# Performance work log

Hardware: AMD Instinct MI355X
Metric: run time of the kernel (lower is better)

The kernel has to match this reference:

```python
import jax, jax.numpy as jnp
import numpy as np

N = 100000   # nodes
E = 200000   # edges
B = 2048     # graphs
D = 256      # embed_dim
L = 5        # gnn layers
NUM_ATOM = 500
NUM_CHI = 500
NUM_BOND_TYPE = 5
NUM_BOND_DIR = 3
BN_EPS = 1e-5


def setup_inputs() -> dict:
    key = jax.random.key(0)
    ks = jax.random.split(key, 20)

    def xavier(k, shape):
        fan_in, fan_out = shape[-2], shape[-1]
        lim = float(np.sqrt(6.0 / (fan_in + fan_out)))
        return jax.random.uniform(k, shape, jnp.float32, -lim, lim)

    inp = {}
    inp["x"] = jax.random.randint(ks[0], (N, 2), 0, NUM_CHI, dtype=jnp.int32)
    inp["edge_index"] = jax.random.randint(ks[1], (2, E), 0, N, dtype=jnp.int32)
    inp["edge_attr"] = jax.random.randint(ks[2], (E, 2), 0, NUM_BOND_DIR, dtype=jnp.int32)
    inp["batch"] = jnp.sort(jax.random.randint(ks[3], (N,), 0, B, dtype=jnp.int32))

    # node embeddings
    inp["x_emb1"] = xavier(ks[4], (NUM_ATOM, D))
    inp["x_emb2"] = xavier(ks[5], (NUM_CHI, D))
    # per-layer edge embeddings (stacked over L layers)
    inp["edge_emb1"] = xavier(ks[6], (L, NUM_BOND_TYPE, D))
    inp["edge_emb2"] = xavier(ks[7], (L, NUM_BOND_DIR, D))
    # per-layer GINE MLP: Linear(D, 2D) -> ReLU -> Linear(2D, D)
    inp["W1"] = xavier(ks[8], (L, D, 2 * D))
    inp["b1"] = jnp.zeros((L, 2 * D), jnp.float32)
    inp["W2"] = xavier(ks[9], (L, 2 * D, D))
    inp["b2"] = jnp.zeros((L, D), jnp.float32)
    # per-layer BatchNorm affine params
    inp["bn_g"] = jnp.ones((L, D), jnp.float32)
    inp["bn_b"] = jnp.zeros((L, D), jnp.float32)
    # output head: Linear(D, D//2) -> Softplus -> Linear(D//2, 2)
    inp["Wo1"] = xavier(ks[10], (D, D // 2))
    inp["bo1"] = jnp.zeros((D // 2,), jnp.float32)
    inp["Wo2"] = xavier(ks[11], (D // 2, 2))
    inp["bo2"] = jnp.zeros((2,), jnp.float32)
    return inp


def reference(x, edge_index, edge_attr, batch,
              x_emb1, x_emb2, edge_emb1, edge_emb2,
              W1, b1, W2, b2, bn_g, bn_b,
              Wo1, bo1, Wo2, bo2):
    n = x.shape[0]
    src, dst = edge_index[0], edge_index[1]
    bt, bd = edge_attr[:, 0], edge_attr[:, 1]

    # initial node features
    h = x_emb1[x[:, 0]] + x_emb2[x[:, 1]]  # [N, D]

    for l in range(L):
        # edge embeddings for real edges
        e = edge_emb1[l][bt] + edge_emb2[l][bd]          # [E, D]
        # self-loop edges carry attr (4, 0)
        self_e = edge_emb1[l][4] + edge_emb2[l][0]       # [D]
        # message = x_j + edge_attr, scatter-add to destination; self-loops add h + self_e
        agg = jax.ops.segment_sum(h[src] + e, dst, num_segments=n) + h + self_e
        # GINE update MLP
        z = jax.nn.relu(agg @ W1[l] + b1[l]) @ W2[l] + b2[l]
        # BatchNorm1d (training-mode batch statistics, biased variance)
        mu = z.mean(axis=0)
        var = z.var(axis=0)
        z = (z - mu) / jnp.sqrt(var + BN_EPS) * bn_g[l] + bn_b[l]
        h = jax.nn.relu(z)  # dropout=0 -> identity

    # global mean pool over graphs
    cnt = jax.ops.segment_sum(jnp.ones((n,), h.dtype), batch, num_segments=B)
    pooled = jax.ops.segment_sum(h, batch, num_segments=B) / jnp.maximum(cnt, 1.0)[:, None]

    # output head (y.size(0) != 2 so proj_head is skipped)
    out = jax.nn.softplus(pooled @ Wo1 + bo1) @ Wo2 + bo2  # [B, 2]
    return out
```

## Files before the change

kernel.cpp:

```cpp
#include <hip/hip_runtime.h>

#define NNODES 100000
#define NEDGES 200000
#define NB     2048
#define DIM    256
#define NLAYERS 5
#define NSB    98

typedef __bf16 bf16x8 __attribute__((ext_vector_type(8)));
typedef float  f32x4  __attribute__((ext_vector_type(4)));

__device__ __forceinline__ float bf2f(unsigned short u) {
    union { unsigned u; float f; } v; v.u = ((unsigned)u) << 16; return v.f;
}
__device__ __forceinline__ unsigned short f2bf(float f) {
    union { float f; unsigned u; } v; v.f = f;
    unsigned r = v.u + 0x7fff + ((v.u >> 16) & 1);
    return (unsigned short)(r >> 16);
}
__device__ __forceinline__ float4 loadZ4(const unsigned short* z, size_t row, int ch) {
    ushort4 u = *(const ushort4*)&z[row * DIM + ch];
    float4 r; r.x = bf2f(u.x); r.y = bf2f(u.y); r.z = bf2f(u.z); r.w = bf2f(u.w); return r;
}

__global__ void zero_i32(int* __restrict__ p, int n) {
    int i = blockIdx.x * 256 + threadIdx.x;
    if (i < n) p[i] = 0;
}

__global__ void transpose_w(const float* __restrict__ W,
                            unsigned short* __restrict__ Wt, int K, int Nw) {
    int l = blockIdx.y;
    int t = blockIdx.x * 256 + threadIdx.x;
    int total = K * Nw;
    if (t >= total) return;
    int k = t / Nw, n = t % Nw;
    Wt[(size_t)l * total + (size_t)n * K + k] = f2bf(W[(size_t)l * total + t]);
}

__global__ void build_etab(const float* __restrict__ ee1, const float* __restrict__ ee2,
                           float* __restrict__ etab) {
    int l = blockIdx.y, c = blockIdx.x, d = threadIdx.x;
    etab[((size_t)l * 15 + c) * DIM + d] =
        ee1[((size_t)l * 5 + c / 3) * DIM + d] + ee2[((size_t)l * 3 + c % 3) * DIM + d];
}

__global__ void csr_hist(const int* __restrict__ ei, int* __restrict__ deg) {
    int j = blockIdx.x * 256 + threadIdx.x;
    if (j < NEDGES) atomicAdd(&deg[ei[NEDGES + j]], 1);
}
__global__ __launch_bounds__(1024) void scan_blk(const int* __restrict__ deg,
                                                 int* __restrict__ rowptr,
                                                 int* __restrict__ bsum) {
    __shared__ int s[1024];
    int b = blockIdx.x, t = threadIdx.x, i = b * 1024 + t;
    s[t] = (i < NNODES) ? deg[i] : 0;
    __syncthreads();
    #pragma unroll
    for (int off = 1; off < 1024; off <<= 1) {
        int u = (t >= off) ? s[t - off] : 0;
        __syncthreads();
        s[t] += u;
        __syncthreads();
    }
    if (i < NNODES) rowptr[i + 1] = s[t];
    if (t == 1023) bsum[b] = s[1023];
}
__global__ void scan_partials(int* __restrict__ bsum) {
    if (threadIdx.x == 0) {
        int acc = 0;
        for (int k = 0; k < NSB; ++k) { acc += bsum[k]; bsum[k] = acc; }
    }
}
__global__ void scan_add(int* __restrict__ rowptr, const int* __restrict__ bsum) {
    int b = blockIdx.x, t = threadIdx.x, i = b * 1024 + t;
    if (b > 0 && i < NNODES) rowptr[i + 1] += bsum[b - 1];
    if (b == 0 && t == 0) rowptr[0] = 0;
}
__global__ void csr_fill(const int* __restrict__ ei, const int* __restrict__ ea,
                         const int* __restrict__ rowptr, int* __restrict__ deg,
                         int* __restrict__ esrc, int* __restrict__ eattr) {
    int j = blockIdx.x * 256 + threadIdx.x;
    if (j >= NEDGES) return;
    int d = ei[NEDGES + j];
    int pos = atomicSub(&deg[d], 1) - 1;
    int slot = rowptr[d] + pos;
    esrc[slot] = ei[j];
    eattr[slot] = ea[2 * j] * 3 + ea[2 * j + 1];
}

__global__ void seg_starts(const int* __restrict__ batch, int* __restrict__ start) {
    int g = blockIdx.x * 256 + threadIdx.x;
    if (g > NB) return;
    int lo = 0, hi = NNODES;
    while (lo < hi) { int mid = (lo + hi) >> 1; if (batch[mid] < g) lo = mid + 1; else hi = mid; }
    start[g] = lo;
}

template <int MODE>
__global__ __launch_bounds__(256) void gather_k(const unsigned short* __restrict__ z,
                                                const int* __restrict__ x,
                                                const float* __restrict__ xe1,
                                                const float* __restrict__ xe2,
                                                const float* __restrict__ statsP,
                                                const float* __restrict__ g_,
                                                const float* __restrict__ b_,
                                                float* __restrict__ statsZ,
                                                const float* __restrict__ etab_l,
                                                const int* __restrict__ rowptr,
                                                const int* __restrict__ esrc,
                                                const int* __restrict__ eattr,
                                                unsigned short* __restrict__ agg) {
    if (blockIdx.x == 0) { statsZ[threadIdx.x] = 0.f; statsZ[256 + threadIdx.x] = 0.f; }
    int i = blockIdx.x * 4 + (threadIdx.x >> 6);
    int lane = threadIdx.x & 63, ch = lane * 4;

    float4 a4, c4;
    if (MODE == 1) {
        float4 s4 = *(const float4*)&statsP[ch];
        float4 q4 = *(const float4*)&statsP[256 + ch];
        float4 g4 = *(const float4*)&g_[ch];
        float4 b4 = *(const float4*)&b_[ch];
        const float invN = 1.0f / (float)NNODES;
        float mux = s4.x * invN, muy = s4.y * invN, muz = s4.z * invN, muw = s4.w * invN;
        a4.x = g4.x * rsqrtf(q4.x * invN - mux * mux + 1e-5f);
        a4.y = g4.y * rsqrtf(q4.y * invN - muy * muy + 1e-5f);
        a4.z = g4.z * rsqrtf(q4.z * invN - muz * muz + 1e-5f);
        a4.w = g4.w * rsqrtf(q4.w * invN - muw * muw + 1e-5f);
        c4.x = b4.x - mux * a4.x; c4.y = b4.y - muy * a4.y;
        c4.z = b4.z - muz * a4.z; c4.w = b4.w - muw * a4.w;
    }

    auto hrow = [&](int row) -> float4 {
        if (MODE == 0) {
            int i0 = x[2 * row], i1 = x[2 * row + 1];
            float4 u = *(const float4*)&xe1[(size_t)i0 * DIM + ch];
            float4 v = *(const float4*)&xe2[(size_t)i1 * DIM + ch];
            return make_float4(u.x + v.x, u.y + v.y, u.z + v.z, u.w + v.w);
        } else {
            float4 h = loadZ4(z, (size_t)row, ch);
            h.x = fmaxf(h.x * a4.x + c4.x, 0.f); h.y = fmaxf(h.y * a4.y + c4.y, 0.f);
            h.z = fmaxf(h.z * a4.z + c4.z, 0.f); h.w = fmaxf(h.w * a4.w + c4.w, 0.f);
            return h;
        }
    };

    float4 se = *(const float4*)&etab_l[12 * DIM + ch];
    float4 hv = hrow(i);
    float4 acc = make_float4(hv.x + se.x, hv.y + se.y, hv.z + se.z, hv.w + se.w);

    int r0 = rowptr[i], r1 = rowptr[i + 1];
    int e = r0;
    for (; e + 2 <= r1; e += 2) {
        int s0 = esrc[e], c0 = eattr[e];
        int s1 = esrc[e + 1], c1 = eattr[e + 1];
        float4 h0 = hrow(s0);
        float4 h1 = hrow(s1);
        float4 e0 = *(const float4*)&etab_l[c0 * DIM + ch];
        float4 e1 = *(const float4*)&etab_l[c1 * DIM + ch];
        acc.x += h0.x + e0.x + h1.x + e1.x; acc.y += h0.y + e0.y + h1.y + e1.y;
        acc.z += h0.z + e0.z + h1.z + e1.z; acc.w += h0.w + e0.w + h1.w + e1.w;
    }
    if (e < r1) {
        int s0 = esrc[e], c0 = eattr[e];
        float4 h0 = hrow(s0);
        float4 e0 = *(const float4*)&etab_l[c0 * DIM + ch];
        acc.x += h0.x + e0.x; acc.y += h0.y + e0.y;
        acc.z += h0.z + e0.z; acc.w += h0.w + e0.w;
    }
    ushort4 o; o.x = f2bf(acc.x); o.y = f2bf(acc.y); o.z = f2bf(acc.z); o.w = f2bf(acc.w);
    *(ushort4*)&agg[(size_t)i * DIM + ch] = o;
}

__global__ __launch_bounds__(512, 6) void mlp64(const unsigned short* __restrict__ agg,
                                                const unsigned short* __restrict__ Wt1,
                                                const float* __restrict__ b1,
                                                const unsigned short* __restrict__ Wt2,
                                                const float* __restrict__ b2,
                                                unsigned short* __restrict__ z,
                                                float* __restrict__ stats) {
    __shared__ unsigned short As[64 * 264];
    __shared__ unsigned short Ts[64 * 136];

    const int rowBase = blockIdx.x * 64;
    const int tid = threadIdx.x;
    const int lane = tid & 63, w = tid >> 6;
    const int lrow = lane & 15, lq = lane >> 4;

    #pragma unroll
    for (int c = tid; c < 64 * 32; c += 512) {
        int r = c >> 5, cc = c & 31;
        int row = rowBase + r; if (row >= NNODES) row = NNODES - 1;
        *(uint4*)&As[r * 264 + cc * 8] = *(const uint4*)&agg[(size_t)row * DIM + cc * 8];
    }
    f32x4 acc2[4][2]{};
    __syncthreads();

    #pragma unroll
    for (int q = 0; q < 4; ++q) {
        f32x4 acc1[4]{};
        const unsigned short* w1p = &Wt1[(size_t)(q * 128 + w * 16 + lrow) * DIM];
        #pragma unroll
        for (int kk = 0; kk < 8; ++kk) {
            const int kc = kk * 32 + lq * 8;
            bf16x8 b = *(const bf16x8*)&w1p[kc];
            bf16x8 a[4];
            #pragma unroll
            for (int mi = 0; mi < 4; ++mi)
                a[mi] = *(const bf16x8*)&As[(mi * 16 + lrow) * 264 + kc];
            #pragma unroll
            for (int mi = 0; mi < 4; ++mi)
                acc1[mi] = __builtin_amdgcn_mfma_f32_16x16x32_bf16(a[mi], b, acc1[mi], 0, 0, 0);
        }
        if (q > 0) __syncthreads();
        {
            int col = w * 16 + lrow;
            float bv = b1[q * 128 + col];
            #pragma unroll
            for (int mi = 0; mi < 4; ++mi)
                #pragma unroll
                for (int r = 0; r < 4; ++r)
                    Ts[(mi * 16 + lq * 4 + r) * 136 + col] = f2bf(fmaxf(acc1[mi][r] + bv, 0.f));
        }
        __syncthreads();
        #pragma unroll
        for (int kk = 0; kk < 4; ++kk) {
            const int kc = kk * 32 + lq * 8;
            bf16x8 a[4], b[2];
            #pragma unroll
            for (int mi = 0; mi < 4; ++mi)
                a[mi] = *(const bf16x8*)&Ts[(mi * 16 + lrow) * 136 + kc];
            #pragma unroll
            for (int ni = 0; ni < 2; ++ni)
                b[ni] = *(const bf16x8*)&Wt2[(size_t)(w * 32 + ni * 16 + lrow) * (2 * DIM) + q * 128 + kc];
            #pragma unroll
            for (int mi = 0; mi < 4; ++mi)
                #pragma unroll
                for (int ni = 0; ni < 2; ++ni)
                    acc2[mi][ni] = __builtin_amdgcn_mfma_f32_16x16x32_bf16(a[mi], b[ni], acc2[mi][ni], 0, 0, 0);
        }
    }

    #pragma unroll
    for (int ni = 0; ni < 2; ++ni) {
        int col = w * 32 + ni * 16 + lrow;
        float bv = b2[col];
        float s = 0.f, q = 0.f;
        #pragma unroll
        for (int mi = 0; mi < 4; ++mi)
            #pragma unroll
            for (int r = 0; r < 4; ++r) {
                int row = rowBase + mi * 16 + lq * 4 + r;
                if (row < NNODES) {
                    float v = acc2[mi][ni][r] + bv;
                    z[(size_t)row * DIM + col] = f2bf(v);
                    s += v; q += v * v;
                }
            }
        s += __shfl_xor(s, 16); s += __shfl_xor(s, 32);
        q += __shfl_xor(q, 16); q += __shfl_xor(q, 32);
        if (lq == 0) {
            atomicAdd(&stats[col], s);
            atomicAdd(&stats[DIM + col], q);
        }
    }
}

__global__ __launch_bounds__(256) void pool_seg(const unsigned short* __restrict__ z,
                                                const float* __restrict__ statsP,
                                                const float* __restrict__ g_,
                                                const float* __restrict__ b_,
                                                const int* __restrict__ start,
                                                float* __restrict__ pooled) {
    int g = blockIdx.x, ch = threadIdx.x;
    float mu = statsP[ch] / (float)NNODES;
    float var = statsP[256 + ch] / (float)NNODES - mu * mu;
    float a = g_[ch] * rsqrtf(var + 1e-5f);
    float c = b_[ch] - mu * a;
    int r0 = start[g], r1 = start[g + 1];
    float s = 0.f;
    for (int i = r0; i < r1; ++i)
        s += fmaxf(bf2f(z[(size_t)i * DIM + ch]) * a + c, 0.f);
    pooled[(size_t)g * DIM + ch] = s / fmaxf((float)(r1 - r0), 1.f);
}

__global__ __launch_bounds__(128) void head_mlp(const float* __restrict__ pooled,
                                                const float* __restrict__ Wo1,
                                                const float* __restrict__ bo1,
                                                const float* __restrict__ Wo2,
                                                const float* __restrict__ bo2,
                                                float* __restrict__ out) {
    __shared__ float p[DIM];
    __shared__ float r0[128], r1[128];
    int g = blockIdx.x, j = threadIdx.x;
    for (int k = j; k < DIM; k += 128) p[k] = pooled[(size_t)g * DIM + k];
    __syncthreads();
    float acc = bo1[j];
    for (int k = 0; k < DIM; ++k) acc += p[k] * Wo1[k * 128 + j];
    float sp = (acc > 20.f) ? acc : log1pf(expf(acc));
    r0[j] = sp * Wo2[j * 2 + 0];
    r1[j] = sp * Wo2[j * 2 + 1];
    __syncthreads();
    for (int s = 64; s > 0; s >>= 1) {
        if (j < s) { r0[j] += r0[j + s]; r1[j] += r1[j + s]; }
        __syncthreads();
    }
    if (j == 0) {
        out[g * 2 + 0] = r0[0] + bo2[0];
        out[g * 2 + 1] = r1[0] + bo2[1];
    }
}

extern "C" void kernel_launch(void* const* d_in, const int* in_sizes, int n_in,
                              void* d_out, int out_size, void* d_ws, size_t ws_size,
                              hipStream_t stream) {
    (void)in_sizes; (void)n_in; (void)out_size;
    const int* x     = (const int*)d_in[0];
    const int* ei    = (const int*)d_in[1];
    const int* ea    = (const int*)d_in[2];
    const int* batch = (const int*)d_in[3];
    const float* xe1 = (const float*)d_in[4];
    const float* xe2 = (const float*)d_in[5];
    const float* ee1 = (const float*)d_in[6];
    const float* ee2 = (const float*)d_in[7];
    const float* W1  = (const float*)d_in[8];
    const float* b1  = (const float*)d_in[9];
    const float* W2  = (const float*)d_in[10];
    const float* b2  = (const float*)d_in[11];
    const float* bng = (const float*)d_in[12];
    const float* bnb = (const float*)d_in[13];
    const float* Wo1 = (const float*)d_in[14];
    const float* bo1 = (const float*)d_in[15];
    const float* Wo2 = (const float*)d_in[16];
    const float* bo2 = (const float*)d_in[17];
    float* out = (float*)d_out;

    if (ws_size < 112000000ull) return;

    char* ws = (char*)d_ws;
    size_t off = 0;
    auto alloc = [&](size_t bytes) { void* p = ws + off; off += (bytes + 255) & ~255ull; return p; };
    unsigned short* z   = (unsigned short*)alloc((size_t)NNODES * DIM * 2);
    unsigned short* agg = (unsigned short*)alloc((size_t)NNODES * DIM * 2);
    unsigned short* Wt1 = (unsigned short*)alloc((size_t)NLAYERS * DIM * 2 * DIM * 2);
    unsigned short* Wt2 = (unsigned short*)alloc((size_t)NLAYERS * DIM * 2 * DIM * 2);
    float* etab         = (float*)alloc((size_t)NLAYERS * 15 * DIM * 4);
    float* stats        = (float*)alloc(2 * 512 * 4);
    float* pooled       = (float*)alloc((size_t)NB * DIM * 4);
    int* gstart         = (int*)alloc((size_t)(NB + 1) * 4);
    int* rowptr         = (int*)alloc((size_t)(NNODES + 1) * 4);
    int* deg            = (int*)alloc((size_t)NNODES * 4);
    int* esrc           = (int*)alloc((size_t)NEDGES * 4);
    int* eattr          = (int*)alloc((size_t)NEDGES * 4);
    int* bsum           = (int*)alloc((size_t)NSB * 4);

    const int WTOT = DIM * 2 * DIM;

    transpose_w<<<dim3((WTOT + 255) / 256, NLAYERS), 256, 0, stream>>>(W1, Wt1, DIM, 2 * DIM);
    transpose_w<<<dim3((WTOT + 255) / 256, NLAYERS), 256, 0, stream>>>(W2, Wt2, 2 * DIM, DIM);
    build_etab<<<dim3(15, NLAYERS), DIM, 0, stream>>>(ee1, ee2, etab);

    zero_i32<<<(NNODES + 255) / 256, 256, 0, stream>>>(deg, NNODES);
    csr_hist<<<(NEDGES + 255) / 256, 256, 0, stream>>>(ei, deg);
    scan_blk<<<NSB, 1024, 0, stream>>>(deg, rowptr, bsum);
    scan_partials<<<1, 64, 0, stream>>>(bsum);
    scan_add<<<NSB, 1024, 0, stream>>>(rowptr, bsum);
    csr_fill<<<(NEDGES + 255) / 256, 256, 0, stream>>>(ei, ea, rowptr, deg, esrc, eattr);
    seg_starts<<<(NB + 1 + 255) / 256, 256, 0, stream>>>(batch, gstart);

    for (int l = 0; l < NLAYERS; ++l) {
        float* statsP = stats + ((l + 1) & 1) * 512;
        float* statsC = stats + (l & 1) * 512;
        if (l == 0)
            gather_k<0><<<NNODES / 4, 256, 0, stream>>>(z, x, xe1, xe2, statsP, bng, bnb, statsC,
                                                        etab, rowptr, esrc, eattr, agg);
        else
            gather_k<1><<<NNODES / 4, 256, 0, stream>>>(z, x, xe1, xe2, statsP,
                                                        bng + (size_t)(l - 1) * DIM, bnb + (size_t)(l - 1) * DIM,
                                                        statsC, etab + (size_t)l * 15 * DIM,
                                                        rowptr, esrc, eattr, agg);
        mlp64<<<(NNODES + 63) / 64, 512, 0, stream>>>(agg, Wt1 + (size_t)l * WTOT, b1 + l * 2 * DIM,
                                                      Wt2 + (size_t)l * WTOT, b2 + l * DIM, z, statsC);
    }

    pool_seg<<<NB, DIM, 0, stream>>>(z, stats + ((NLAYERS - 1) & 1) * 512,
                                     bng + (size_t)(NLAYERS - 1) * DIM, bnb + (size_t)(NLAYERS - 1) * DIM,
                                     gstart, pooled);
    head_mlp<<<NB, 128, 0, stream>>>(pooled, Wo1, bo1, Wo2, bo2, out);
}
```

Before: 1.101 ms.

## Fuse neighbor gather into MLP kernel with ping-pong node buffers

Merges the per-layer gather/aggregate kernel into the MLP kernel. Each 512-thread block now aggregates its 64 rows straight into shared memory instead of writing and re-reading a bf16 agg buffer. Node features ping-pong between two buffers, because one layer's gathers read the previous z while other blocks write the new z. Stats use a 3-slot rotation so the slot being zeroed, read and accumulated never collide. This removes one full N×D round trip through memory and one launch per layer, but the gather now runs at the MLP kernel's occupancy and cannot overlap with the GEMM phase inside a block.

```diff
diff --git a/kernel.cpp b/kernel.cpp
--- a/kernel.cpp
+++ b/kernel.cpp
@@ -26,6 +26,10 @@
 __global__ void zero_i32(int* __restrict__ p, int n) {
     int i = blockIdx.x * 256 + threadIdx.x;
     if (i < n) p[i] = 0;
+}
+__global__ void zero_f32(float* __restrict__ p, int n) {
+    int i = blockIdx.x * 256 + threadIdx.x;
+    if (i < n) p[i] = 0.f;
 }
 
 __global__ void transpose_w(const float* __restrict__ W,
@@ -98,87 +102,24 @@
 }
 
 template <int MODE>
-__global__ __launch_bounds__(256) void gather_k(const unsigned short* __restrict__ z,
-                                                const int* __restrict__ x,
-                                                const float* __restrict__ xe1,
-                                                const float* __restrict__ xe2,
-                                                const float* __restrict__ statsP,
-                                                const float* __restrict__ g_,
-                                                const float* __restrict__ b_,
-                                                float* __restrict__ statsZ,
-                                                const float* __restrict__ etab_l,
-                                                const int* __restrict__ rowptr,
-                                                const int* __restrict__ esrc,
-                                                const int* __restrict__ eattr,
-                                                unsigned short* __restrict__ agg) {
-    if (blockIdx.x == 0) { statsZ[threadIdx.x] = 0.f; statsZ[256 + threadIdx.x] = 0.f; }
-    int i = blockIdx.x * 4 + (threadIdx.x >> 6);
-    int lane = threadIdx.x & 63, ch = lane * 4;
-
-    float4 a4, c4;
-    if (MODE == 1) {
-        float4 s4 = *(const float4*)&statsP[ch];
-        float4 q4 = *(const float4*)&statsP[256 + ch];
-        float4 g4 = *(const float4*)&g_[ch];
-        float4 b4 = *(const float4*)&b_[ch];
-        const float invN = 1.0f / (float)NNODES;
-        float mux = s4.x * invN, muy = s4.y * invN, muz = s4.z * invN, muw = s4.w * invN;
-        a4.x = g4.x * rsqrtf(q4.x * invN - mux * mux + 1e-5f);
-        a4.y = g4.y * rsqrtf(q4.y * invN - muy * muy + 1e-5f);
-        a4.z = g4.z * rsqrtf(q4.z * invN - muz * muz + 1e-5f);
-        a4.w = g4.w * rsqrtf(q4.w * invN - muw * muw + 1e-5f);
-        c4.x = b4.x - mux * a4.x; c4.y = b4.y - muy * a4.y;
-        c4.z = b4.z - muz * a4.z; c4.w = b4.w - muw * a4.w;
-    }
-
-    auto hrow = [&](int row) -> float4 {
-        if (MODE == 0) {
-            int i0 = x[2 * row], i1 = x[2 * row + 1];
-            float4 u = *(const float4*)&xe1[(size_t)i0 * DIM + ch];
-            float4 v = *(const float4*)&xe2[(size_t)i1 * DIM + ch];
-            return make_float4(u.x + v.x, u.y + v.y, u.z + v.z, u.w + v.w);
-        } else {
-            float4 h = loadZ4(z, (size_t)row, ch);
-            h.x = fmaxf(h.x * a4.x + c4.x, 0.f); h.y = fmaxf(h.y * a4.y + c4.y, 0.f);
-            h.z = fmaxf(h.z * a4.z + c4.z, 0.f); h.w = fmaxf(h.w * a4.w + c4.w, 0.f);
-            return h;
-        }
-    };
-
-    float4 se = *(const float4*)&etab_l[12 * DIM + ch];
-    float4 hv = hrow(i);
-    float4 acc = make_float4(hv.x + se.x, hv.y + se.y, hv.z + se.z, hv.w + se.w);
-
-    int r0 = rowptr[i], r1 = rowptr[i + 1];
-    int e = r0;
-    for (; e + 2 <= r1; e += 2) {
-        int s0 = esrc[e], c0 = eattr[e];
-        int s1 = esrc[e + 1], c1 = eattr[e + 1];
-        float4 h0 = hrow(s0);
-        float4 h1 = hrow(s1);
-        float4 e0 = *(const float4*)&etab_l[c0 * DIM + ch];
-        float4 e1 = *(const float4*)&etab_l[c1 * DIM + ch];
-        acc.x += h0.x + e0.x + h1.x + e1.x; acc.y += h0.y + e0.y + h1.y + e1.y;
-        acc.z += h0.z + e0.z + h1.z + e1.z; acc.w += h0.w + e0.w + h1.w + e1.w;
-    }
-    if (e < r1) {
-        int s0 = esrc[e], c0 = eattr[e];
-        float4 h0 = hrow(s0);
-        float4 e0 = *(const float4*)&etab_l[c0 * DIM + ch];
-        acc.x += h0.x + e0.x; acc.y += h0.y + e0.y;
-        acc.z += h0.z + e0.z; acc.w += h0.w + e0.w;
-    }
-    ushort4 o; o.x = f2bf(acc.x); o.y = f2bf(acc.y); o.z = f2bf(acc.z); o.w = f2bf(acc.w);
-    *(ushort4*)&agg[(size_t)i * DIM + ch] = o;
-}
-
-__global__ __launch_bounds__(512, 6) void mlp64(const unsigned short* __restrict__ agg,
-                                                const unsigned short* __restrict__ Wt1,
-                                                const float* __restrict__ b1,
-                                                const unsigned short* __restrict__ Wt2,
-                                                const float* __restrict__ b2,
-                                                unsigned short* __restrict__ z,
-                                                float* __restrict__ stats) {
+__global__ __launch_bounds__(512, 6) void layer_k(const unsigned short* __restrict__ zsrc,
+                                                  unsigned short* __restrict__ zdst,
+                                                  const int* __restrict__ x,
+                                                  const float* __restrict__ xe1,
+                                                  const float* __restrict__ xe2,
+                                                  const float* __restrict__ statsP,
+                                                  float* __restrict__ statsZ,
+                                                  const float* __restrict__ g_,
+                                                  const float* __restrict__ b_,
+                                                  const float* __restrict__ etab_l,
+                                                  const int* __restrict__ rowptr,
+                                                  const int* __restrict__ esrc,
+                                                  const int* __restrict__ eattr,
+                                                  const unsigned short* __restrict__ Wt1,
+                                                  const float* __restrict__ b1,
+                                                  const unsigned short* __restrict__ Wt2,
+                                                  const float* __restrict__ b2,
+                                                  float* __restrict__ stats) {
     __shared__ unsigned short As[64 * 264];
     __shared__ unsigned short Ts[64 * 136];
 
@@ -187,11 +128,69 @@
     const int lane = tid & 63, w = tid >> 6;
     const int lrow = lane & 15, lq = lane >> 4;
 
-    #pragma unroll
-    for (int c = tid; c < 64 * 32; c += 512) {
-        int r = c >> 5, cc = c & 31;
-        int row = rowBase + r; if (row >= NNODES) row = NNODES - 1;
-        *(uint4*)&As[r * 264 + cc * 8] = *(const uint4*)&agg[(size_t)row * DIM + cc * 8];
+    if (blockIdx.x == 0 && tid < 512) statsZ[tid] = 0.f;
+
+    {
+        const int ch = lane * 4;
+        float4 a4, c4;
+        if (MODE == 1) {
+            float4 s4 = *(const float4*)&statsP[ch];
+            float4 q4 = *(const float4*)&statsP[256 + ch];
+            float4 g4 = *(const float4*)&g_[ch];
+            float4 b4 = *(const float4*)&b_[ch];
+            const float invN = 1.0f / (float)NNODES;
+            float mux = s4.x * invN, muy = s4.y * invN, muz = s4.z * invN, muw = s4.w * invN;
+            a4.x = g4.x * rsqrtf(q4.x * invN - mux * mux + 1e-5f);
+            a4.y = g4.y * rsqrtf(q4.y * invN - muy * muy + 1e-5f);
+            a4.z = g4.z * rsqrtf(q4.z * invN - muz * muz + 1e-5f);
+            a4.w = g4.w * rsqrtf(q4.w * invN - muw * muw + 1e-5f);
+            c4.x = b4.x - mux * a4.x; c4.y = b4.y - muy * a4.y;
+            c4.z = b4.z - muz * a4.z; c4.w = b4.w - muw * a4.w;
+        }
+        auto hrow = [&](int row) -> float4 {
+            if (MODE == 0) {
+                int i0 = x[2 * row], i1 = x[2 * row + 1];
+                float4 u = *(const float4*)&xe1[(size_t)i0 * DIM + ch];
+                float4 v = *(const float4*)&xe2[(size_t)i1 * DIM + ch];
+                return make_float4(u.x + v.x, u.y + v.y, u.z + v.z, u.w + v.w);
+            } else {
+                float4 h = loadZ4(zsrc, (size_t)row, ch);
+                h.x = fmaxf(h.x * a4.x + c4.x, 0.f); h.y = fmaxf(h.y * a4.y + c4.y, 0.f);
+                h.z = fmaxf(h.z * a4.z + c4.z, 0.f); h.w = fmaxf(h.w * a4.w + c4.w, 0.f);
+                return h;
+            }
+        };
+        float4 se = *(const float4*)&etab_l[12 * DIM + ch];
+        #pragma unroll
+        for (int r8 = 0; r8 < 8; ++r8) {
+            int row = rowBase + w * 8 + r8;
+            float4 acc = make_float4(0.f, 0.f, 0.f, 0.f);
+            if (row < NNODES) {
+                float4 hv = hrow(row);
+                acc = make_float4(hv.x + se.x, hv.y + se.y, hv.z + se.z, hv.w + se.w);
+                int r0 = rowptr[row], r1 = rowptr[row + 1];
+                int e = r0;
+                for (; e + 2 <= r1; e += 2) {
+                    int s0 = esrc[e], c0 = eattr[e];
+                    int s1 = esrc[e + 1], c1 = eattr[e + 1];
+                    float4 h0 = hrow(s0);
+                    float4 h1 = hrow(s1);
+                    float4 e0 = *(const float4*)&etab_l[c0 * DIM + ch];
+                    float4 e1 = *(const float4*)&etab_l[c1 * DIM + ch];
+                    acc.x += h0.x + e0.x + h1.x + e1.x; acc.y += h0.y + e0.y + h1.y + e1.y;
+                    acc.z += h0.z + e0.z + h1.z + e1.z; acc.w += h0.w + e0.w + h1.w + e1.w;
+                }
+                if (e < r1) {
+                    int s0 = esrc[e], c0 = eattr[e];
+                    float4 h0 = hrow(s0);
+                    float4 e0 = *(const float4*)&etab_l[c0 * DIM + ch];
+                    acc.x += h0.x + e0.x; acc.y += h0.y + e0.y;
+                    acc.z += h0.z + e0.z; acc.w += h0.w + e0.w;
+                }
+            }
+            ushort4 o; o.x = f2bf(acc.x); o.y = f2bf(acc.y); o.z = f2bf(acc.z); o.w = f2bf(acc.w);
+            *(ushort4*)&As[(w * 8 + r8) * 264 + ch] = o;
+        }
     }
     f32x4 acc2[4][2]{};
     __syncthreads();
@@ -253,7 +252,7 @@
                 int row = rowBase + mi * 16 + lq * 4 + r;
                 if (row < NNODES) {
                     float v = acc2[mi][ni][r] + bv;
-                    z[(size_t)row * DIM + col] = f2bf(v);
+                    zdst[(size_t)row * DIM + col] = f2bf(v);
                     s += v; q += v * v;
                 }
             }
@@ -340,12 +339,12 @@
     char* ws = (char*)d_ws;
     size_t off = 0;
     auto alloc = [&](size_t bytes) { void* p = ws + off; off += (bytes + 255) & ~255ull; return p; };
-    unsigned short* z   = (unsigned short*)alloc((size_t)NNODES * DIM * 2);
-    unsigned short* agg = (unsigned short*)alloc((size_t)NNODES * DIM * 2);
+    unsigned short* zA  = (unsigned short*)alloc((size_t)NNODES * DIM * 2);
+    unsigned short* zB  = (unsigned short*)alloc((size_t)NNODES * DIM * 2);
     unsigned short* Wt1 = (unsigned short*)alloc((size_t)NLAYERS * DIM * 2 * DIM * 2);
     unsigned short* Wt2 = (unsigned short*)alloc((size_t)NLAYERS * DIM * 2 * DIM * 2);
     float* etab         = (float*)alloc((size_t)NLAYERS * 15 * DIM * 4);
-    float* stats        = (float*)alloc(2 * 512 * 4);
+    float* stats        = (float*)alloc(3 * 512 * 4);
     float* pooled       = (float*)alloc((size_t)NB * DIM * 4);
     int* gstart         = (int*)alloc((size_t)(NB + 1) * 4);
     int* rowptr         = (int*)alloc((size_t)(NNODES + 1) * 4);
@@ -355,10 +354,12 @@
     int* bsum           = (int*)alloc((size_t)NSB * 4);
 
     const int WTOT = DIM * 2 * DIM;
+    unsigned short* zb[2] = { zA, zB };
 
     transpose_w<<<dim3((WTOT + 255) / 256, NLAYERS), 256, 0, stream>>>(W1, Wt1, DIM, 2 * DIM);
     transpose_w<<<dim3((WTOT + 255) / 256, NLAYERS), 256, 0, stream>>>(W2, Wt2, 2 * DIM, DIM);
     build_etab<<<dim3(15, NLAYERS), DIM, 0, stream>>>(ee1, ee2, etab);
+    zero_f32<<<2, 256, 0, stream>>>(stats, 512);
 
     zero_i32<<<(NNODES + 255) / 256, 256, 0, stream>>>(deg, NNODES);
     csr_hist<<<(NEDGES + 255) / 256, 256, 0, stream>>>(ei, deg);
@@ -368,22 +369,24 @@
     csr_fill<<<(NEDGES + 255) / 256, 256, 0, stream>>>(ei, ea, rowptr, deg, esrc, eattr);
     seg_starts<<<(NB + 1 + 255) / 256, 256, 0, stream>>>(batch, gstart);
 
+    const int NBLK = (NNODES + 63) / 64;
     for (int l = 0; l < NLAYERS; ++l) {
-        float* statsP = stats + ((l + 1) & 1) * 512;
-        float* statsC = stats + (l & 1) * 512;
+        float* statsC = stats + (size_t)(l % 3) * 512;
+        float* statsP = stats + (size_t)((l + 2) % 3) * 512;
+        float* statsZ = stats + (size_t)((l + 1) % 3) * 512;
         if (l == 0)
-            gather_k<0><<<NNODES / 4, 256, 0, stream>>>(z, x, xe1, xe2, statsP, bng, bnb, statsC,
-                                                        etab, rowptr, esrc, eattr, agg);
+            layer_k<0><<<NBLK, 512, 0, stream>>>(zb[0], zb[1], x, xe1, xe2, statsP, statsZ,
+                                                 bng, bnb, etab, rowptr, esrc, eattr,
+                                                 Wt1, b1, Wt2, b2, statsC);
         else
-            gather_k<1><<<NNODES / 4, 256, 0, stream>>>(z, x, xe1, xe2, statsP,
-                                                        bng + (size_t)(l - 1) * DIM, bnb + (size_t)(l - 1) * DIM,
-                                                        statsC, etab + (size_t)l * 15 * DIM,
-                                                        rowptr, esrc, eattr, agg);
-        mlp64<<<(NNODES + 63) / 64, 512, 0, stream>>>(agg, Wt1 + (size_t)l * WTOT, b1 + l * 2 * DIM,
-                                                      Wt2 + (size_t)l * WTOT, b2 + l * DIM, z, statsC);
-    }
-
-    pool_seg<<<NB, DIM, 0, stream>>>(z, stats + ((NLAYERS - 1) & 1) * 512,
+            layer_k<1><<<NBLK, 512, 0, stream>>>(zb[l & 1], zb[(l + 1) & 1], x, xe1, xe2, statsP, statsZ,
+                                                 bng + (size_t)(l - 1) * DIM, bnb + (size_t)(l - 1) * DIM,
+                                                 etab + (size_t)l * 15 * DIM, rowptr, esrc, eattr,
+                                                 Wt1 + (size_t)l * WTOT, b1 + (size_t)l * 2 * DIM,
+                                                 Wt2 + (size_t)l * WTOT, b2 + (size_t)l * DIM, statsC);
+    }
+
+    pool_seg<<<NB, DIM, 0, stream>>>(zb[NLAYERS & 1], stats + (size_t)((NLAYERS - 1) % 3) * 512,
                                      bng + (size_t)(NLAYERS - 1) * DIM, bnb + (size_t)(NLAYERS - 1) * DIM,
                                      gstart, pooled);
     head_mlp<<<NB, 128, 0, stream>>>(pooled, Wo1, bo1, Wo2, bo2, out);
```

Measured after the change: 1.056 ms. 1.04x faster.
